# Kernel tuning notes

Measured on AMD Instinct MI355X. Metric: run time of the kernel, lower is better.

The kernel has to match this reference:

```python
import jax, jax.numpy as jnp
import numpy as np

N = 100000   # nodes
E = 1600000  # edges (avg degree 16)
D = 128      # in_dim


def setup_inputs() -> dict:
    key = jax.random.key(0)
    k = jax.random.split(key, 8)
    h = jax.random.normal(k[0], (N, D), dtype=jnp.float32)
    d = jax.random.uniform(k[1], (N,), dtype=jnp.float32)  # per-node degree norm (e.g. deg^-0.5)
    yes_no = jax.random.uniform(k[2], (E,), dtype=jnp.float32)
    gate_w = jax.random.normal(k[3], (1, 2 * D), dtype=jnp.float32) * (1.414 / np.sqrt(2 * D))
    gate_b = jnp.zeros((1,), dtype=jnp.float32)
    yes_weight = jax.random.uniform(k[4], (), dtype=jnp.float32)
    no_weight = jax.random.uniform(k[5], (), dtype=jnp.float32)
    src = jax.random.randint(k[6], (E,), 0, N, dtype=jnp.int64)
    dst = jax.random.randint(k[7], (E,), 0, N, dtype=jnp.int64)
    return {"h": h, "d": d, "yes_no": yes_no, "gate_w": gate_w, "gate_b": gate_b,
            "yes_weight": yes_weight, "no_weight": no_weight, "src": src, "dst": dst}


def reference(h, d, yes_no, gate_w, gate_b, yes_weight, no_weight, src, dst):
    n, dim = h.shape
    # gate(cat[h_dst, h_src]) == h_dst @ W[:, :D].T + h_src @ W[:, D:].T + b
    # project once per node, then gather per edge (avoids [E, 2D] concat)
    p_dst = h @ gate_w[0, :dim]  # [N]
    p_src = h @ gate_w[0, dim:]  # [N]
    g = jnp.tanh(p_dst[dst] + p_src[src] + gate_b[0])  # [E]
    yn = jnp.tanh(yes_no * yes_weight + (1.0 - yes_no) * no_weight)  # [E]
    e = (g + yn) * 0.5 * d[dst] * d[src]  # [E] (dropout p=0 -> identity)
    m = h[src] * e[:, None]  # [E, D] edge messages
    z = jax.ops.segment_sum(m, dst, num_segments=n)  # [N, D]
    return z
```

## Files before the change

kernel.cpp:

```cpp
#include <hip/hip_runtime.h>

#define D 128
#define CAP 64

__device__ __forceinline__ unsigned short f2bf(float x) {
    unsigned int u = __float_as_uint(x);
    u += 0x7FFFu + ((u >> 16) & 1u);
    return (unsigned short)(u >> 16);
}
__device__ __forceinline__ float bf2f(unsigned short b) {
    return __uint_as_float(((unsigned int)b) << 16);
}

__global__ __launch_bounds__(256) void proj_kernel(const float* __restrict__ h,
                                                   const float* __restrict__ gw,
                                                   const float* __restrict__ dnorm,
                                                   float4* __restrict__ q,
                                                   unsigned short* __restrict__ hb,
                                                   int n_nodes) {
    int node = (int)((blockIdx.x * blockDim.x + threadIdx.x) >> 6);
    int lane = threadIdx.x & 63;
    if (node >= n_nodes) return;
    const float2* hr2 = (const float2*)(h + (size_t)node * D);
    const float2* gw2 = (const float2*)gw;
    float2 hv = hr2[lane];
    float2 wa = gw2[lane];
    float2 wb = gw2[lane + 64];
    ushort2 hvb = make_ushort2(f2bf(hv.x), f2bf(hv.y));
    *(ushort2*)(hb + (size_t)node * D + 2 * lane) = hvb;
    float s1 = hv.x * wa.x + hv.y * wa.y;
    float s2 = hv.x * wb.x + hv.y * wb.y;
    #pragma unroll
    for (int off = 32; off > 0; off >>= 1) {
        s1 += __shfl_down(s1, off, 64);
        s2 += __shfl_down(s2, off, 64);
    }
    if (lane == 0) q[node] = make_float4(s1, s2, dnorm[node], 0.0f);
}

__global__ __launch_bounds__(256) void fill_kernel(const float4* __restrict__ q,
                                                   const float* __restrict__ yes_no,
                                                   const int* __restrict__ src,
                                                   const int* __restrict__ dst,
                                                   const float* __restrict__ gate_b,
                                                   const float* __restrict__ yes_w,
                                                   const float* __restrict__ no_w,
                                                   int* __restrict__ cnt,
                                                   unsigned int* __restrict__ csr,
                                                   int n_edges) {
    int i = blockIdx.x * blockDim.x + threadIdx.x;
    int e0 = 2 * i;
    if (e0 >= n_edges) return;
    float gb = gate_b[0];
    float yw = yes_w[0];
    float nw = no_w[0];
    bool has1 = (e0 + 1) < n_edges;

    int2 sv, tv;
    float2 ynv;
    if (has1) {
        sv = *(const int2*)(src + e0);
        tv = *(const int2*)(dst + e0);
        ynv = *(const float2*)(yes_no + e0);
    } else {
        sv = make_int2(src[e0], 0);
        tv = make_int2(dst[e0], 0);
        ynv = make_float2(yes_no[e0], 0.0f);
    }

    float4 qt0 = q[tv.x];
    float4 qs0 = q[sv.x];
    float4 qt1, qs1;
    if (has1) { qt1 = q[tv.y]; qs1 = q[sv.y]; }

    {
        float g = tanhf(qt0.x + qs0.y + gb);
        float y = tanhf(ynv.x * yw + (1.0f - ynv.x) * nw);
        float ce = (g + y) * 0.5f * qt0.z * qs0.z;
        int qv = (int)rintf(ce * 8191.0f) + 8192;
        unsigned int entry = ((unsigned int)sv.x << 15) | (unsigned int)qv;
        int pos = atomicAdd(&cnt[tv.x], 1);
        if (pos < CAP)
            __builtin_nontemporal_store(entry, &csr[(size_t)tv.x * CAP + pos]);
    }
    if (has1) {
        float g = tanhf(qt1.x + qs1.y + gb);
        float y = tanhf(ynv.y * yw + (1.0f - ynv.y) * nw);
        float ce = (g + y) * 0.5f * qt1.z * qs1.z;
        int qv = (int)rintf(ce * 8191.0f) + 8192;
        unsigned int entry = ((unsigned int)sv.y << 15) | (unsigned int)qv;
        int pos = atomicAdd(&cnt[tv.y], 1);
        if (pos < CAP)
            __builtin_nontemporal_store(entry, &csr[(size_t)tv.y * CAP + pos]);
    }
}

__global__ __launch_bounds__(256) void gather_kernel(const unsigned short* __restrict__ hb,
                                                     const int* __restrict__ cnt,
                                                     const unsigned int* __restrict__ csr,
                                                     float4* __restrict__ z4,
                                                     int n_nodes) {
    int node = (int)((blockIdx.x * blockDim.x + threadIdx.x) >> 5);
    int lane = threadIdx.x & 31;
    if (node >= n_nodes) return;
    int n = cnt[node];
    if (n > CAP) n = CAP;
    const unsigned int* row = csr + (size_t)node * CAP;
    float4 acc = make_float4(0.0f, 0.0f, 0.0f, 0.0f);
    const float inv = 1.0f / 8191.0f;
    int k = 0;
    for (; k + 3 < n; k += 4) {
        unsigned int e0 = row[k], e1 = row[k + 1], e2 = row[k + 2], e3 = row[k + 3];
        float c0 = (float)((int)(e0 & 0x7fffu) - 8192) * inv;
        float c1 = (float)((int)(e1 & 0x7fffu) - 8192) * inv;
        float c2 = (float)((int)(e2 & 0x7fffu) - 8192) * inv;
        float c3 = (float)((int)(e3 & 0x7fffu) - 8192) * inv;
        ushort4 a = *(const ushort4*)(hb + (size_t)(e0 >> 15) * D + 4 * lane);
        ushort4 b = *(const ushort4*)(hb + (size_t)(e1 >> 15) * D + 4 * lane);
        ushort4 c = *(const ushort4*)(hb + (size_t)(e2 >> 15) * D + 4 * lane);
        ushort4 d = *(const ushort4*)(hb + (size_t)(e3 >> 15) * D + 4 * lane);
        acc.x += bf2f(a.x) * c0 + bf2f(b.x) * c1 + bf2f(c.x) * c2 + bf2f(d.x) * c3;
        acc.y += bf2f(a.y) * c0 + bf2f(b.y) * c1 + bf2f(c.y) * c2 + bf2f(d.y) * c3;
        acc.z += bf2f(a.z) * c0 + bf2f(b.z) * c1 + bf2f(c.z) * c2 + bf2f(d.z) * c3;
        acc.w += bf2f(a.w) * c0 + bf2f(b.w) * c1 + bf2f(c.w) * c2 + bf2f(d.w) * c3;
    }
    for (; k < n; ++k) {
        unsigned int e0 = row[k];
        float c0 = (float)((int)(e0 & 0x7fffu) - 8192) * inv;
        ushort4 a = *(const ushort4*)(hb + (size_t)(e0 >> 15) * D + 4 * lane);
        acc.x += bf2f(a.x) * c0;
        acc.y += bf2f(a.y) * c0;
        acc.z += bf2f(a.z) * c0;
        acc.w += bf2f(a.w) * c0;
    }
    z4[(size_t)node * (D / 4) + lane] = acc;
}

extern "C" void kernel_launch(void* const* d_in, const int* in_sizes, int n_in,
                              void* d_out, int out_size, void* d_ws, size_t ws_size,
                              hipStream_t stream) {
    const float* h       = (const float*)d_in[0];
    const float* dnorm   = (const float*)d_in[1];
    const float* yes_no  = (const float*)d_in[2];
    const float* gate_w  = (const float*)d_in[3];
    const float* gate_b  = (const float*)d_in[4];
    const float* yes_w   = (const float*)d_in[5];
    const float* no_w    = (const float*)d_in[6];
    const int*   src     = (const int*)d_in[7];
    const int*   dst     = (const int*)d_in[8];

    int n_nodes = in_sizes[0] / D;
    int n_edges = in_sizes[2];

    char* ws = (char*)d_ws;
    size_t off = 0;
    auto take = [&](size_t bytes) {
        void* ptr = ws + off;
        off += (bytes + 15) & ~(size_t)15;
        return ptr;
    };
    float4*         q   = (float4*)take((size_t)n_nodes * sizeof(float4));
    unsigned short* hb  = (unsigned short*)take((size_t)n_nodes * D * sizeof(unsigned short));
    int*            cnt = (int*)take((size_t)n_nodes * sizeof(int));
    unsigned int*   csr = (unsigned int*)take((size_t)n_nodes * CAP * sizeof(unsigned int));
    (void)ws_size;

    hipMemsetAsync(cnt, 0, (size_t)n_nodes * sizeof(int), stream);

    proj_kernel<<<(n_nodes + 3) / 4, 256, 0, stream>>>(h, gate_w, dnorm, q, hb, n_nodes);

    int nt = (n_edges + 1) / 2;
    fill_kernel<<<(nt + 255) / 256, 256, 0, stream>>>(
        q, yes_no, src, dst, gate_b, yes_w, no_w, cnt, csr, n_edges);

    gather_kernel<<<(n_nodes + 7) / 8, 256, 0, stream>>>(
        hb, cnt, csr, (float4*)d_out, n_nodes);
}
```

Baseline: 284.9 us.

## Partition edge fill by destination node range and fold counter reset into projection

```diff
diff --git a/kernel.cpp b/kernel.cpp
--- a/kernel.cpp
+++ b/kernel.cpp
@@ -2,6 +2,10 @@
 
 #define D 128
 #define CAP 64
+#define NPART 8
+
+typedef int   i4v __attribute__((ext_vector_type(4)));
+typedef float f4v __attribute__((ext_vector_type(4)));
 
 __device__ __forceinline__ unsigned short f2bf(float x) {
     unsigned int u = __float_as_uint(x);
@@ -17,6 +21,7 @@
                                                    const float* __restrict__ dnorm,
                                                    float4* __restrict__ q,
                                                    unsigned short* __restrict__ hb,
+                                                   int* __restrict__ cnt,
                                                    int n_nodes) {
     int node = (int)((blockIdx.x * blockDim.x + threadIdx.x) >> 6);
     int lane = threadIdx.x & 63;
@@ -35,63 +40,75 @@
         s1 += __shfl_down(s1, off, 64);
         s2 += __shfl_down(s2, off, 64);
     }
-    if (lane == 0) q[node] = make_float4(s1, s2, dnorm[node], 0.0f);
+    if (lane == 0) {
+        q[node] = make_float4(s1, s2, dnorm[node], 0.0f);
+        cnt[node] = 0;
+    }
 }
 
-__global__ __launch_bounds__(256) void fill_kernel(const float4* __restrict__ q,
-                                                   const float* __restrict__ yes_no,
-                                                   const int* __restrict__ src,
-                                                   const int* __restrict__ dst,
-                                                   const float* __restrict__ gate_b,
-                                                   const float* __restrict__ yes_w,
-                                                   const float* __restrict__ no_w,
-                                                   int* __restrict__ cnt,
-                                                   unsigned int* __restrict__ csr,
-                                                   int n_edges) {
-    int i = blockIdx.x * blockDim.x + threadIdx.x;
-    int e0 = 2 * i;
-    if (e0 >= n_edges) return;
+__device__ __forceinline__ void emit_edge(int d, int s, float yn,
+                                          const float4& qt, const float4& qs,
+                                          float gb, float yw, float nw,
+                                          int* __restrict__ cnt,
+                                          unsigned int* __restrict__ csr) {
+    float g = tanhf(qt.x + qs.y + gb);
+    float y = tanhf(yn * yw + (1.0f - yn) * nw);
+    float ce = (g + y) * 0.5f * qt.z * qs.z;
+    int qv = (int)rintf(ce * 8191.0f) + 8192;
+    unsigned int entry = ((unsigned int)s << 15) | (unsigned int)qv;
+    int pos = atomicAdd(&cnt[d], 1);
+    if (pos < CAP)
+        csr[(size_t)d * CAP + pos] = entry;
+}
+
+__global__ __launch_bounds__(256) void fill_part_kernel(const float4* __restrict__ q,
+                                                        const float* __restrict__ yes_no,
+                                                        const int* __restrict__ src,
+                                                        const int* __restrict__ dst,
+                                                        const float* __restrict__ gate_b,
+                                                        const float* __restrict__ yes_w,
+                                                        const float* __restrict__ no_w,
+                                                        int* __restrict__ cnt,
+                                                        unsigned int* __restrict__ csr,
+                                                        int n_edges, int node_chunk) {
+    int p   = blockIdx.x & (NPART - 1);
+    int cb  = blockIdx.x >> 3;
+    int ncb = gridDim.x >> 3;
+    int lo = p * node_chunk;
+    int hi = lo + node_chunk;
     float gb = gate_b[0];
     float yw = yes_w[0];
     float nw = no_w[0];
-    bool has1 = (e0 + 1) < n_edges;
-
-    int2 sv, tv;
-    float2 ynv;
-    if (has1) {
-        sv = *(const int2*)(src + e0);
-        tv = *(const int2*)(dst + e0);
-        ynv = *(const float2*)(yes_no + e0);
-    } else {
-        sv = make_int2(src[e0], 0);
-        tv = make_int2(dst[e0], 0);
-        ynv = make_float2(yes_no[e0], 0.0f);
+    int nq = n_edges >> 2;
+    for (int i = cb * (int)blockDim.x + (int)threadIdx.x; i < nq; i += ncb * (int)blockDim.x) {
+        i4v dv = __builtin_nontemporal_load((const i4v*)dst + i);
+        bool a0 = (dv.x >= lo) & (dv.x < hi);
+        bool a1 = (dv.y >= lo) & (dv.y < hi);
+        bool a2 = (dv.z >= lo) & (dv.z < hi);
+        bool a3 = (dv.w >= lo) & (dv.w < hi);
+        if (!(a0 | a1 | a2 | a3)) continue;
+        i4v sv = __builtin_nontemporal_load((const i4v*)src + i);
+        f4v yv = __builtin_nontemporal_load((const f4v*)yes_no + i);
+        float4 qt0, qs0, qt1, qs1, qt2, qs2, qt3, qs3;
+        if (a0) { qt0 = q[dv.x]; qs0 = q[sv.x]; }
+        if (a1) { qt1 = q[dv.y]; qs1 = q[sv.y]; }
+        if (a2) { qt2 = q[dv.z]; qs2 = q[sv.z]; }
+        if (a3) { qt3 = q[dv.w]; qs3 = q[sv.w]; }
+        if (a0) emit_edge(dv.x, sv.x, yv.x, qt0, qs0, gb, yw, nw, cnt, csr);
+        if (a1) emit_edge(dv.y, sv.y, yv.y, qt1, qs1, gb, yw, nw, cnt, csr);
+        if (a2) emit_edge(dv.z, sv.z, yv.z, qt2, qs2, gb, yw, nw, cnt, csr);
+        if (a3) emit_edge(dv.w, sv.w, yv.w, qt3, qs3, gb, yw, nw, cnt, csr);
     }
-
-    float4 qt0 = q[tv.x];
-    float4 qs0 = q[sv.x];
-    float4 qt1, qs1;
-    if (has1) { qt1 = q[tv.y]; qs1 = q[sv.y]; }
-
-    {
-        float g = tanhf(qt0.x + qs0.y + gb);
-        float y = tanhf(ynv.x * yw + (1.0f - ynv.x) * nw);
-        float ce = (g + y) * 0.5f * qt0.z * qs0.z;
-        int qv = (int)rintf(ce * 8191.0f) + 8192;
-        unsigned int entry = ((unsigned int)sv.x << 15) | (unsigned int)qv;
-        int pos = atomicAdd(&cnt[tv.x], 1);
-        if (pos < CAP)
-            __builtin_nontemporal_store(entry, &csr[(size_t)tv.x * CAP + pos]);
-    }
-    if (has1) {
-        float g = tanhf(qt1.x + qs1.y + gb);
-        float y = tanhf(ynv.y * yw + (1.0f - ynv.y) * nw);
-        float ce = (g + y) * 0.5f * qt1.z * qs1.z;
-        int qv = (int)rintf(ce * 8191.0f) + 8192;
-        unsigned int entry = ((unsigned int)sv.y << 15) | (unsigned int)qv;
-        int pos = atomicAdd(&cnt[tv.y], 1);
-        if (pos < CAP)
-            __builtin_nontemporal_store(entry, &csr[(size_t)tv.y * CAP + pos]);
+    int t0 = nq << 2;
+    if (cb == 0 && (int)threadIdx.x < (n_edges - t0)) {
+        int e = t0 + (int)threadIdx.x;
+        int dd = dst[e];
+        if (dd >= lo && dd < hi) {
+            int ss = src[e];
+            float4 qt = q[dd];
+            float4 qs = q[ss];
+            emit_edge(dd, ss, yes_no[e], qt, qs, gb, yw, nw, cnt, csr);
+        }
     }
 }
 
@@ -165,13 +182,11 @@
     unsigned int*   csr = (unsigned int*)take((size_t)n_nodes * CAP * sizeof(unsigned int));
     (void)ws_size;
 
-    hipMemsetAsync(cnt, 0, (size_t)n_nodes * sizeof(int), stream);
+    proj_kernel<<<(n_nodes + 3) / 4, 256, 0, stream>>>(h, gate_w, dnorm, q, hb, cnt, n_nodes);
 
-    proj_kernel<<<(n_nodes + 3) / 4, 256, 0, stream>>>(h, gate_w, dnorm, q, hb, n_nodes);
-
-    int nt = (n_edges + 1) / 2;
-    fill_kernel<<<(nt + 255) / 256, 256, 0, stream>>>(
-        q, yes_no, src, dst, gate_b, yes_w, no_w, cnt, csr, n_edges);
+    int node_chunk = (n_nodes + NPART - 1) / NPART;
+    fill_part_kernel<<<2048, 256, 0, stream>>>(
+        q, yes_no, src, dst, gate_b, yes_w, no_w, cnt, csr, n_edges, node_chunk);
 
     gather_kernel<<<(n_nodes + 7) / 8, 256, 0, stream>>>(
         hb, cnt, csr, (float4*)d_out, n_nodes);
```

Measured after the change: 296.5 us. 4.1% more time.

## Replace global-atomic CSR fill with two-pass LDS binning by destination bucket

Applied to the files above, without the earlier changes.

```diff
diff --git a/kernel.cpp b/kernel.cpp
--- a/kernel.cpp
+++ b/kernel.cpp
@@ -2,6 +2,10 @@
 
 #define D 128
 #define CAP 64
+#define NPB 250
+#define NBMAX 512
+#define EPB 4096
+#define BCAP 5120
 
 __device__ __forceinline__ unsigned short f2bf(float x) {
     unsigned int u = __float_as_uint(x);
@@ -17,7 +21,12 @@
                                                    const float* __restrict__ dnorm,
                                                    float4* __restrict__ q,
                                                    unsigned short* __restrict__ hb,
+                                                   unsigned int* __restrict__ tails,
                                                    int n_nodes) {
+    if (blockIdx.x == 0) {
+        tails[threadIdx.x] = 0u;
+        tails[threadIdx.x + 256] = 0u;
+    }
     int node = (int)((blockIdx.x * blockDim.x + threadIdx.x) >> 6);
     int lane = threadIdx.x & 63;
     if (node >= n_nodes) return;
@@ -38,61 +47,150 @@
     if (lane == 0) q[node] = make_float4(s1, s2, dnorm[node], 0.0f);
 }
 
-__global__ __launch_bounds__(256) void fill_kernel(const float4* __restrict__ q,
-                                                   const float* __restrict__ yes_no,
-                                                   const int* __restrict__ src,
-                                                   const int* __restrict__ dst,
-                                                   const float* __restrict__ gate_b,
-                                                   const float* __restrict__ yes_w,
-                                                   const float* __restrict__ no_w,
-                                                   int* __restrict__ cnt,
-                                                   unsigned int* __restrict__ csr,
-                                                   int n_edges) {
-    int i = blockIdx.x * blockDim.x + threadIdx.x;
-    int e0 = 2 * i;
-    if (e0 >= n_edges) return;
+__global__ __launch_bounds__(512) void bin_kernel(const float4* __restrict__ q,
+                                                  const float* __restrict__ yes_no,
+                                                  const int* __restrict__ src,
+                                                  const int* __restrict__ dst,
+                                                  const float* __restrict__ gate_b,
+                                                  const float* __restrict__ yes_w,
+                                                  const float* __restrict__ no_w,
+                                                  unsigned int* __restrict__ tails,
+                                                  unsigned long long* __restrict__ recs,
+                                                  int n_edges, int nb) {
+    __shared__ unsigned long long sorted[EPB];
+    __shared__ unsigned int hist[NBMAX];
+    __shared__ unsigned int sbuf[NBMAX];
+    __shared__ unsigned int base[NBMAX];
+    __shared__ unsigned int cursor[NBMAX];
+    __shared__ unsigned int gbase[NBMAX];
+
+    int tid = threadIdx.x;
+    int e0 = blockIdx.x * EPB;
+    int n = n_edges - e0;
+    if (n > EPB) n = EPB;
+
+    hist[tid] = 0u;
+    __syncthreads();
+
+    for (int j = tid; j < n; j += 512) {
+        unsigned int d = (unsigned int)dst[e0 + j];
+        atomicAdd(&hist[d / NPB], 1u);
+    }
+    __syncthreads();
+
+    sbuf[tid] = hist[tid];
+    __syncthreads();
+    unsigned int* pa = sbuf;
+    unsigned int* pb = gbase;
+    #pragma unroll
+    for (int s = 1; s < NBMAX; s <<= 1) {
+        unsigned int v = pa[tid] + ((tid >= s) ? pa[tid - s] : 0u);
+        pb[tid] = v;
+        __syncthreads();
+        unsigned int* t = pa; pa = pb; pb = t;
+    }
+    unsigned int ex = (tid == 0) ? 0u : pa[tid - 1];
+    base[tid] = ex;
+    cursor[tid] = ex;
+    __syncthreads();
+
     float gb = gate_b[0];
     float yw = yes_w[0];
     float nw = no_w[0];
-    bool has1 = (e0 + 1) < n_edges;
-
-    int2 sv, tv;
-    float2 ynv;
-    if (has1) {
-        sv = *(const int2*)(src + e0);
-        tv = *(const int2*)(dst + e0);
-        ynv = *(const float2*)(yes_no + e0);
-    } else {
-        sv = make_int2(src[e0], 0);
-        tv = make_int2(dst[e0], 0);
-        ynv = make_float2(yes_no[e0], 0.0f);
-    }
-
-    float4 qt0 = q[tv.x];
-    float4 qs0 = q[sv.x];
-    float4 qt1, qs1;
-    if (has1) { qt1 = q[tv.y]; qs1 = q[sv.y]; }
-
-    {
-        float g = tanhf(qt0.x + qs0.y + gb);
-        float y = tanhf(ynv.x * yw + (1.0f - ynv.x) * nw);
-        float ce = (g + y) * 0.5f * qt0.z * qs0.z;
+
+    for (int j = tid; j < n; j += 512) {
+        int e = e0 + j;
+        int dd = dst[e];
+        int ss = src[e];
+        float yn = yes_no[e];
+        float4 qt = q[dd];
+        float4 qs = q[ss];
+        float g = tanhf(qt.x + qs.y + gb);
+        float y = tanhf(yn * yw + (1.0f - yn) * nw);
+        float ce = (g + y) * 0.5f * qt.z * qs.z;
         int qv = (int)rintf(ce * 8191.0f) + 8192;
-        unsigned int entry = ((unsigned int)sv.x << 15) | (unsigned int)qv;
-        int pos = atomicAdd(&cnt[tv.x], 1);
-        if (pos < CAP)
-            __builtin_nontemporal_store(entry, &csr[(size_t)tv.x * CAP + pos]);
-    }
-    if (has1) {
-        float g = tanhf(qt1.x + qs1.y + gb);
-        float y = tanhf(ynv.y * yw + (1.0f - ynv.y) * nw);
-        float ce = (g + y) * 0.5f * qt1.z * qs1.z;
-        int qv = (int)rintf(ce * 8191.0f) + 8192;
-        unsigned int entry = ((unsigned int)sv.y << 15) | (unsigned int)qv;
-        int pos = atomicAdd(&cnt[tv.y], 1);
-        if (pos < CAP)
-            __builtin_nontemporal_store(entry, &csr[(size_t)tv.y * CAP + pos]);
-    }
+        unsigned int w0 = ((unsigned int)ss << 15) | (unsigned int)qv;
+        unsigned int bk = (unsigned int)dd / NPB;
+        unsigned int pos = atomicAdd(&cursor[bk], 1u);
+        sorted[pos] = ((unsigned long long)(unsigned int)dd << 32) | (unsigned long long)w0;
+    }
+    __syncthreads();
+
+    gbase[tid] = (hist[tid] > 0u) ? atomicAdd(&tails[tid], hist[tid]) : 0u;
+    __syncthreads();
+
+    for (int j = tid; j < n; j += 512) {
+        unsigned long long r = sorted[j];
+        unsigned int bk = (unsigned int)(r >> 32) / NPB;
+        unsigned int gpos = gbase[bk] + ((unsigned int)j - base[bk]);
+        if (gpos < BCAP)
+            __builtin_nontemporal_store(r, recs + (size_t)bk * BCAP + gpos);
+    }
+}
+
+__global__ __launch_bounds__(256) void scatter_kernel(const unsigned int* __restrict__ tails,
+                                                      const unsigned long long* __restrict__ recs,
+                                                      int* __restrict__ cnt,
+                                                      unsigned int* __restrict__ csr,
+                                                      int n_nodes) {
+    __shared__ unsigned int sw0[BCAP];
+    __shared__ unsigned char snl[BCAP];
+    __shared__ unsigned int hist2[256];
+    __shared__ unsigned int sa[256];
+    __shared__ unsigned int sb[256];
+    __shared__ unsigned int rowbase[256];
+    __shared__ unsigned int cursor2[256];
+
+    int b = blockIdx.x;
+    int tid = threadIdx.x;
+    unsigned int nrec = tails[b];
+    if (nrec > BCAP) nrec = BCAP;
+    const unsigned long long* rb = recs + (size_t)b * BCAP;
+    int node0 = b * NPB;
+
+    hist2[tid] = 0u;
+    __syncthreads();
+
+    for (unsigned int j = tid; j < nrec; j += 256) {
+        unsigned long long r = __builtin_nontemporal_load(rb + j);
+        unsigned int nl = (unsigned int)(r >> 32) - (unsigned int)node0;
+        atomicAdd(&hist2[nl], 1u);
+    }
+    __syncthreads();
+
+    sa[tid] = hist2[tid];
+    __syncthreads();
+    unsigned int* pa = sa;
+    unsigned int* pb = sb;
+    #pragma unroll
+    for (int s = 1; s < 256; s <<= 1) {
+        unsigned int v = pa[tid] + ((tid >= s) ? pa[tid - s] : 0u);
+        pb[tid] = v;
+        __syncthreads();
+        unsigned int* t = pa; pa = pb; pb = t;
+    }
+    unsigned int ex = (tid == 0) ? 0u : pa[tid - 1];
+    rowbase[tid] = ex;
+    cursor2[tid] = ex;
+    __syncthreads();
+
+    for (unsigned int j = tid; j < nrec; j += 256) {
+        unsigned long long r = rb[j];
+        unsigned int nl = (unsigned int)(r >> 32) - (unsigned int)node0;
+        unsigned int pos = atomicAdd(&cursor2[nl], 1u);
+        sw0[pos] = (unsigned int)r;
+        snl[pos] = (unsigned char)nl;
+    }
+    __syncthreads();
+
+    for (unsigned int j = tid; j < nrec; j += 256) {
+        unsigned int nl = snl[j];
+        unsigned int k = j - rowbase[nl];
+        if (k < CAP)
+            csr[(size_t)(node0 + (int)nl) * CAP + k] = sw0[j];
+    }
+    if (tid < NPB && node0 + tid < n_nodes)
+        cnt[node0 + tid] = (int)hist2[tid];
 }
 
 __global__ __launch_bounds__(256) void gather_kernel(const unsigned short* __restrict__ hb,
@@ -151,6 +249,7 @@
 
     int n_nodes = in_sizes[0] / D;
     int n_edges = in_sizes[2];
+    int nb = (n_nodes + NPB - 1) / NPB;
 
     char* ws = (char*)d_ws;
     size_t off = 0;
@@ -159,19 +258,20 @@
         off += (bytes + 15) & ~(size_t)15;
         return ptr;
     };
-    float4*         q   = (float4*)take((size_t)n_nodes * sizeof(float4));
-    unsigned short* hb  = (unsigned short*)take((size_t)n_nodes * D * sizeof(unsigned short));
-    int*            cnt = (int*)take((size_t)n_nodes * sizeof(int));
-    unsigned int*   csr = (unsigned int*)take((size_t)n_nodes * CAP * sizeof(unsigned int));
+    float4*             q     = (float4*)take((size_t)n_nodes * sizeof(float4));
+    unsigned short*     hb    = (unsigned short*)take((size_t)n_nodes * D * sizeof(unsigned short));
+    int*                cnt   = (int*)take((size_t)n_nodes * sizeof(int));
+    unsigned int*       csr   = (unsigned int*)take((size_t)n_nodes * CAP * sizeof(unsigned int));
+    unsigned int*       tails = (unsigned int*)take((size_t)NBMAX * sizeof(unsigned int));
+    unsigned long long* recs  = (unsigned long long*)take((size_t)nb * BCAP * sizeof(unsigned long long));
     (void)ws_size;
 
-    hipMemsetAsync(cnt, 0, (size_t)n_nodes * sizeof(int), stream);
-
-    proj_kernel<<<(n_nodes + 3) / 4, 256, 0, stream>>>(h, gate_w, dnorm, q, hb, n_nodes);
-
-    int nt = (n_edges + 1) / 2;
-    fill_kernel<<<(nt + 255) / 256, 256, 0, stream>>>(
-        q, yes_no, src, dst, gate_b, yes_w, no_w, cnt, csr, n_edges);
+    proj_kernel<<<(n_nodes + 3) / 4, 256, 0, stream>>>(h, gate_w, dnorm, q, hb, tails, n_nodes);
+
+    bin_kernel<<<(n_edges + EPB - 1) / EPB, 512, 0, stream>>>(
+        q, yes_no, src, dst, gate_b, yes_w, no_w, tails, recs, n_edges, nb);
+
+    scatter_kernel<<<nb, 256, 0, stream>>>(tails, recs, cnt, csr, n_nodes);
 
     gather_kernel<<<(n_nodes + 7) / 8, 256, 0, stream>>>(
         hb, cnt, csr, (float4*)d_out, n_nodes);
```

Result: faster. 259.6 us (-8.9%).
